# Kernel optimization log

Measured on AMD Instinct MI355X. Metric: run time of the kernel, lower is better.

The kernel has to match this reference:

```python
import jax, jax.numpy as jnp
from jax import lax
import numpy as np

EPS = 1e-5
ALPHA = 0.2  # LeakyReLU slope


def setup_inputs() -> dict:
    key = jax.random.key(0)
    ks = jax.random.split(key, 8)
    B, N, F_IN, HID, OUT, H = 32, 512, 256, 512, 512, 4
    D = OUT // H
    return {
        "x": jax.random.normal(ks[0], (B, N, F_IN), dtype=jnp.float32),
        "adj": jax.random.uniform(ks[1], (N, N), dtype=jnp.float32),
        "gc_w": jax.random.normal(ks[2], (F_IN, HID), dtype=jnp.float32) * 0.04,
        "gc_b": jax.random.normal(ks[3], (HID,), dtype=jnp.float32) * 0.04,
        "bn1_g": jnp.ones((HID,), jnp.float32),
        "bn1_b": jnp.zeros((HID,), jnp.float32),
        "bn1_m": jnp.zeros((HID,), jnp.float32),
        "bn1_v": jnp.ones((HID,), jnp.float32),
        "gat_w": jax.random.normal(ks[4], (H, D, HID), dtype=jnp.float32) * 0.04,
        "conv_w": jax.random.normal(ks[5], (OUT, OUT, 3), dtype=jnp.float32) * 0.02,
        "conv_b": jax.random.normal(ks[6], (OUT,), dtype=jnp.float32) * 0.02,
        "bn2_g": jnp.ones((OUT,), jnp.float32),
        "bn2_b": jnp.zeros((OUT,), jnp.float32),
        "bn2_m": jnp.zeros((OUT,), jnp.float32),
        "bn2_v": jnp.ones((OUT,), jnp.float32),
    }


def reference(x, adj, gc_w, gc_b, bn1_g, bn1_b, bn1_m, bn1_v, gat_w,
              conv_w, conv_b, bn2_g, bn2_b, bn2_m, bn2_v):
    # --- GraphConvolution: adj @ (x @ W) + b ---
    support = jnp.einsum('bnc,cd->bnd', x, gc_w)
    g = jnp.einsum('nm,bmd->bnd', adj, support) + gc_b  # [B,N,HID]
    # --- BatchNorm1d over channel dim (eval mode) + ReLU ---
    g = (g - bn1_m) * (bn1_g / jnp.sqrt(bn1_v + EPS)) + bn1_b
    g = jax.nn.relu(g)
    # --- Multi-head GAT (repeat/mul/sum == attention-weighted matmul) ---
    hh = jnp.einsum('bnf,hdf->bhnd', g, gat_w)           # per-head projections
    e = jnp.einsum('bhnd,bhmd->bhnm', hh, hh)            # logits [B,H,N,N]
    e = jnp.where(e > 0, e, ALPHA * e)                   # LeakyReLU
    att = jax.nn.softmax(e, axis=-1)
    o = jnp.einsum('bhnm,bhmd->bhnd', att, hh)
    B, H, N, D = o.shape
    o = o.transpose(0, 2, 1, 3).reshape(B, N, H * D)     # concat heads [B,N,OUT]
    # --- TCN block: conv1d(k=3,pad=1) over node axis + BN(eval) + ReLU ---
    xc = o.transpose(0, 2, 1)                            # [B,C,N]
    y = lax.conv_general_dilated(xc, conv_w, (1,), ((1, 1),),
                                 dimension_numbers=('NCH', 'OIH', 'NCH'))
    y = y + conv_b[None, :, None]
    y = (y - bn2_m[None, :, None]) * (bn2_g / jnp.sqrt(bn2_v + EPS))[None, :, None] + bn2_b[None, :, None]
    y = jax.nn.relu(y)
    return y.transpose(0, 2, 1)                          # [B,N,OUT]
```

## Files before the change

kernel.cpp:

```cpp
#include <hip/hip_runtime.h>
#include <math.h>

#define BATCH 32
#define NNODE 512
#define FIN   256
#define HIDC  512
#define OUTC  512
#define NHEAD 4
#define HDIM  128
#define EPSV  1e-5f
#define ALPHA_LR 0.2f

typedef _Float16 half8 __attribute__((ext_vector_type(8)));
typedef _Float16 half4v __attribute__((ext_vector_type(4)));
typedef float floatx4 __attribute__((ext_vector_type(4)));

#define GLOBAL_TO_LDS16(g, l)                                                  \
  __builtin_amdgcn_global_load_lds(                                            \
      (const __attribute__((address_space(1))) void*)(g),                      \
      (__attribute__((address_space(3))) void*)(l), 16, 0, 0)

__device__ __forceinline__ void split_gemm_acc(
    const _Float16* __restrict__ Ah, const _Float16* __restrict__ Al, int lda,
    const _Float16* __restrict__ Bh, const _Float16* __restrict__ Bl, int ldb,
    int K, int rowBase, int colBase,
    _Float16* sAh, _Float16* sAl, _Float16* sBh, _Float16* sBl,
    floatx4 acc[4][4], int tid) {
  const int lane = tid & 63, wave = tid >> 6;
  const int wr = (wave >> 1) * 64, wc = (wave & 1) * 64;
  const int fr = lane & 15, q = lane >> 4;
  const int r = tid >> 2, ko = (tid & 3) * 8;
  for (int k0 = 0; k0 < K; k0 += 32) {
    GLOBAL_TO_LDS16(&Ah[(size_t)(rowBase + r) * lda + k0 + ko], &sAh[tid * 8]);
    GLOBAL_TO_LDS16(&Ah[(size_t)(rowBase + r + 64) * lda + k0 + ko], &sAh[2048 + tid * 8]);
    GLOBAL_TO_LDS16(&Al[(size_t)(rowBase + r) * lda + k0 + ko], &sAl[tid * 8]);
    GLOBAL_TO_LDS16(&Al[(size_t)(rowBase + r + 64) * lda + k0 + ko], &sAl[2048 + tid * 8]);
    GLOBAL_TO_LDS16(&Bh[(size_t)(colBase + r) * ldb + k0 + ko], &sBh[tid * 8]);
    GLOBAL_TO_LDS16(&Bh[(size_t)(colBase + r + 64) * ldb + k0 + ko], &sBh[2048 + tid * 8]);
    GLOBAL_TO_LDS16(&Bl[(size_t)(colBase + r) * ldb + k0 + ko], &sBl[tid * 8]);
    GLOBAL_TO_LDS16(&Bl[(size_t)(colBase + r + 64) * ldb + k0 + ko], &sBl[2048 + tid * 8]);
    __syncthreads();
    half8 ah[4], al4[4], bh[4], bl4[4];
#pragma unroll
    for (int i = 0; i < 4; ++i) {
      ah[i]  = *(const half8*)&sAh[(wr + i * 16 + fr) * 32 + q * 8];
      al4[i] = *(const half8*)&sAl[(wr + i * 16 + fr) * 32 + q * 8];
    }
#pragma unroll
    for (int j = 0; j < 4; ++j) {
      bh[j]  = *(const half8*)&sBh[(wc + j * 16 + fr) * 32 + q * 8];
      bl4[j] = *(const half8*)&sBl[(wc + j * 16 + fr) * 32 + q * 8];
    }
#pragma unroll
    for (int i = 0; i < 4; ++i)
#pragma unroll
      for (int j = 0; j < 4; ++j) {
        acc[i][j] = __builtin_amdgcn_mfma_f32_16x16x32_f16(al4[i], bh[j], acc[i][j], 0, 0, 0);
        acc[i][j] = __builtin_amdgcn_mfma_f32_16x16x32_f16(ah[i], bl4[j], acc[i][j], 0, 0, 0);
        acc[i][j] = __builtin_amdgcn_mfma_f32_16x16x32_f16(ah[i], bh[j], acc[i][j], 0, 0, 0);
      }
    __syncthreads();
  }
}

__global__ __launch_bounds__(256) void k_prep(
    const float* __restrict__ adj, const float* __restrict__ gcw,
    const float* __restrict__ gatw, const float* __restrict__ cw,
    _Float16* __restrict__ ADJh, _Float16* __restrict__ ADJl,
    _Float16* __restrict__ GWh, _Float16* __restrict__ GWl,
    _Float16* __restrict__ GAh, _Float16* __restrict__ GAl,
    _Float16* __restrict__ WT, _Float16* __restrict__ OP) {
  const int i = blockIdx.x * 256 + threadIdx.x;
  if (i < 262144) {
    float v = adj[i];
    _Float16 h = (_Float16)v;
    ADJh[i] = h; ADJl[i] = (_Float16)(v - (float)h);
  } else if (i < 393216) {
    int j = i - 262144;
    int n = j >> 8, k = j & 255;
    float v = gcw[(size_t)k * HIDC + n];
    _Float16 h = (_Float16)v;
    GWh[j] = h; GWl[j] = (_Float16)(v - (float)h);
  } else if (i < 655360) {
    int j = i - 393216;
    float v = gatw[j];
    _Float16 h = (_Float16)v;
    GAh[j] = h; GAl[j] = (_Float16)(v - (float)h);
  } else if (i < 1441792) {
    int j = i - 655360;
    int n = j / 1536, kk = j - n * 1536;
    int tap = kk >> 9, ci = kk & 511;
    WT[j] = (_Float16)cw[(size_t)n * 1536 + ci * 3 + tap];
  } else if (i < 1474560) {
    int j = i - 1441792;
    int b = j >> 10, rs = (j >> 9) & 1, c = j & 511;
    OP[((size_t)b * 514 + rs * 513) * OUTC + c] = (_Float16)0.f;
  }
}

__global__ __launch_bounds__(256) void k_xsplit(const float* __restrict__ X,
                                                _Float16* __restrict__ Xh,
                                                _Float16* __restrict__ Xl) {
  const int i = (blockIdx.x * 256 + threadIdx.x) * 4;
  float4 v = *(const float4*)&X[i];
  half4v h, l;
  h[0] = (_Float16)v.x; l[0] = (_Float16)(v.x - (float)h[0]);
  h[1] = (_Float16)v.y; l[1] = (_Float16)(v.y - (float)h[1]);
  h[2] = (_Float16)v.z; l[2] = (_Float16)(v.z - (float)h[2]);
  h[3] = (_Float16)v.w; l[3] = (_Float16)(v.w - (float)h[3]);
  *(half4v*)&Xh[i] = h;
  *(half4v*)&Xl[i] = l;
}

__global__ __launch_bounds__(256) void k_support_t(
    const _Float16* __restrict__ GWh, const _Float16* __restrict__ GWl,
    const _Float16* __restrict__ Xh, const _Float16* __restrict__ Xl,
    _Float16* __restrict__ STh, _Float16* __restrict__ STl) {
  __shared__ _Float16 sm[4][4096];
  const int tid = threadIdx.x;
  const int rowBase = blockIdx.y * 128, colBase = blockIdx.x * 128;
  floatx4 acc[4][4] = {};
  split_gemm_acc(GWh, GWl, FIN, Xh, Xl, FIN, FIN, rowBase, colBase,
                 sm[0], sm[1], sm[2], sm[3], acc, tid);
  const int lane = tid & 63, wave = tid >> 6;
  const int wr = (wave >> 1) * 64, wc = (wave & 1) * 64;
  const int fr = lane & 15, q = lane >> 4;
#pragma unroll
  for (int i = 0; i < 4; ++i) {
    const int ch0 = rowBase + wr + i * 16 + q * 4;
#pragma unroll
    for (int rg = 0; rg < 4; ++rg) {
      size_t base = (size_t)(ch0 + rg) * 16384 + colBase + wc + fr;
#pragma unroll
      for (int j = 0; j < 4; ++j) {
        float v = acc[i][j][rg];
        _Float16 h = (_Float16)v;
        STh[base + j * 16] = h;
        STl[base + j * 16] = (_Float16)(v - (float)h);
      }
    }
  }
}

__global__ __launch_bounds__(256) void k_gcn(
    const _Float16* __restrict__ ADJh, const _Float16* __restrict__ ADJl,
    const _Float16* __restrict__ STh, const _Float16* __restrict__ STl,
    const float* __restrict__ gcb, const float* __restrict__ g1,
    const float* __restrict__ b1, const float* __restrict__ m1,
    const float* __restrict__ v1,
    _Float16* __restrict__ Gh, _Float16* __restrict__ Gl) {
  __shared__ _Float16 sm[4][4096];
  const int tid = threadIdx.x;
  const int rowBase = blockIdx.y * 128, colBase = blockIdx.x * 128;
  const int b = blockIdx.z;
  floatx4 acc[4][4] = {};
  split_gemm_acc(ADJh, ADJl, NNODE, STh + (size_t)b * NNODE, STl + (size_t)b * NNODE,
                 16384, NNODE, rowBase, colBase, sm[0], sm[1], sm[2], sm[3], acc, tid);
  const int lane = tid & 63, wave = tid >> 6;
  const int wr = (wave >> 1) * 64, wc = (wave & 1) * 64;
  const int fr = lane & 15, q = lane >> 4;
  float sc[4], of[4];
#pragma unroll
  for (int j = 0; j < 4; ++j) {
    int c = colBase + wc + j * 16 + fr;
    float s = g1[c] * rsqrtf(v1[c] + EPSV);
    sc[j] = s;
    of[j] = (gcb[c] - m1[c]) * s + b1[c];
  }
#pragma unroll
  for (int i = 0; i < 4; ++i) {
    const int n0 = rowBase + wr + i * 16 + q * 4;
#pragma unroll
    for (int rg = 0; rg < 4; ++rg) {
      size_t base = ((size_t)b * NNODE + n0 + rg) * HIDC + colBase + wc + fr;
#pragma unroll
      for (int j = 0; j < 4; ++j) {
        float v = fmaxf(fmaf(acc[i][j][rg], sc[j], of[j]), 0.0f);
        _Float16 h = (_Float16)v;
        Gh[base + j * 16] = h;
        Gl[base + j * 16] = (_Float16)(v - (float)h);
      }
    }
  }
}

__global__ __launch_bounds__(256) void k_hh(
    const _Float16* __restrict__ Gh, const _Float16* __restrict__ Gl,
    const _Float16* __restrict__ GAh, const _Float16* __restrict__ GAl,
    _Float16* __restrict__ HHh, _Float16* __restrict__ HHl) {
  __shared__ _Float16 sm[4][4096];
  const int tid = threadIdx.x;
  const int rowBase = blockIdx.y * 128, colBase = blockIdx.x * 128;
  floatx4 acc[4][4] = {};
  split_gemm_acc(Gh, Gl, HIDC, GAh, GAl, HIDC, HIDC, rowBase, colBase,
                 sm[0], sm[1], sm[2], sm[3], acc, tid);
  const int lane = tid & 63, wave = tid >> 6;
  const int wr = (wave >> 1) * 64, wc = (wave & 1) * 64;
  const int fr = lane & 15, q = lane >> 4;
#pragma unroll
  for (int i = 0; i < 4; ++i) {
    const int r0 = rowBase + wr + i * 16 + q * 4;
#pragma unroll
    for (int rg = 0; rg < 4; ++rg) {
      size_t base = (size_t)(r0 + rg) * OUTC + colBase + wc + fr;
#pragma unroll
      for (int j = 0; j < 4; ++j) {
        float v = acc[i][j][rg];
        _Float16 h = (_Float16)v;
        HHh[base + j * 16] = h;
        HHl[base + j * 16] = (_Float16)(v - (float)h);
      }
    }
  }
}

__global__ __launch_bounds__(256) void k_vt(const _Float16* __restrict__ HHh,
                                            _Float16* __restrict__ HHT) {
  __shared__ _Float16 sT[128 * 132];
  const int bt = blockIdx.x;
  const int nt = bt & 3, g = bt >> 2;
  const int bb = g >> 2, h = g & 3;
  const int tid = threadIdx.x;
  const int rr = tid >> 4, cc = (tid & 15) * 8;
#pragma unroll
  for (int it = 0; it < 8; ++it) {
    int node = rr + it * 16;
    half8 v = *(const half8*)&HHh[((size_t)bb * 512 + nt * 128 + node) * 512 + h * 128 + cc];
#pragma unroll
    for (int e = 0; e < 8; ++e) sT[(cc + e) * 132 + node] = v[e];
  }
  __syncthreads();
#pragma unroll
  for (int it = 0; it < 8; ++it) {
    int d = rr + it * 16;
    half8 v;
#pragma unroll
    for (int e = 0; e < 8; ++e) v[e] = sT[d * 132 + cc + e];
    *(half8*)&HHT[((size_t)g * 128 + d) * 512 + nt * 128 + cc] = v;
  }
}

__global__ __launch_bounds__(256, 3) void k_attn(
    const _Float16* __restrict__ HHh, const _Float16* __restrict__ HHl,
    const _Float16* __restrict__ HHT, _Float16* __restrict__ OP) {
  __shared__ _Float16 sK[8][2048];
  __shared__ _Float16 sP[64 * 68];
  _Float16* sV = &sK[0][0];
  const int tid = threadIdx.x;
  const int lane = tid & 63, wave = tid >> 6;
  const int fr = lane & 15, q = lane >> 4;
  const int id = blockIdx.x;
  const int slot = id >> 3;
  const int g = (id & 7) + 8 * (slot >> 3);
  const int qBase = (slot & 7) * 64;
  const int bb = g >> 2, h = g & 3;
  const int w16 = wave * 16;
  const _Float16* Qh = HHh + (size_t)bb * NNODE * OUTC + h * HDIM;
  const _Float16* Ql = HHl + (size_t)bb * NNODE * OUTC + h * HDIM;
  const _Float16* VT = HHT + (size_t)g * HDIM * NNODE;
  const int rk = tid >> 2, ck = (tid & 3) * 8;

  half8 qh[4], ql[4];
#pragma unroll
  for (int k0 = 0; k0 < 4; ++k0) {
    const size_t off = (size_t)(qBase + w16 + fr) * OUTC + k0 * 32 + q * 8;
    qh[k0] = *(const half8*)&Qh[off];
    ql[k0] = *(const half8*)&Ql[off];
  }

  floatx4 oacc[8] = {};
  float m_i[4], l_i[4];
#pragma unroll
  for (int rg = 0; rg < 4; ++rg) { m_i[rg] = -1e30f; l_i[rg] = 0.f; }

  for (int kt = 0; kt < 8; ++kt) {
    const int ktb = kt * 64;
#pragma unroll
    for (int t = 0; t < 4; ++t) {
      GLOBAL_TO_LDS16(&Qh[(size_t)(ktb + rk) * OUTC + t * 32 + ck], &sK[t][tid * 8]);
      GLOBAL_TO_LDS16(&Ql[(size_t)(ktb + rk) * OUTC + t * 32 + ck], &sK[4 + t][tid * 8]);
    }
    __syncthreads();
    floatx4 sacc[4] = {};
#pragma unroll
    for (int k0 = 0; k0 < 4; ++k0)
#pragma unroll
      for (int j = 0; j < 4; ++j) {
        half8 bh = *(const half8*)&sK[k0][(j * 16 + fr) * 32 + q * 8];
        half8 bl = *(const half8*)&sK[4 + k0][(j * 16 + fr) * 32 + q * 8];
        sacc[j] = __builtin_amdgcn_mfma_f32_16x16x32_f16(ql[k0], bh, sacc[j], 0, 0, 0);
        sacc[j] = __builtin_amdgcn_mfma_f32_16x16x32_f16(qh[k0], bl, sacc[j], 0, 0, 0);
        sacc[j] = __builtin_amdgcn_mfma_f32_16x16x32_f16(qh[k0], bh, sacc[j], 0, 0, 0);
      }
    __syncthreads();
#pragma unroll
    for (int j = 0; j < 4; ++j)
#pragma unroll
      for (int rg = 0; rg < 4; ++rg) {
        float v = sacc[j][rg];
        sacc[j][rg] = v > 0.f ? v : ALPHA_LR * v;
      }
#pragma unroll
    for (int rg = 0; rg < 4; ++rg) {
      float mx = sacc[0][rg];
#pragma unroll
      for (int j = 1; j < 4; ++j) mx = fmaxf(mx, sacc[j][rg]);
      mx = fmaxf(mx, __shfl_xor(mx, 1));
      mx = fmaxf(mx, __shfl_xor(mx, 2));
      mx = fmaxf(mx, __shfl_xor(mx, 4));
      mx = fmaxf(mx, __shfl_xor(mx, 8));
      float mnew = fmaxf(m_i[rg], mx);
      float alpha = __expf(m_i[rg] - mnew);
      m_i[rg] = mnew;
      float sum = 0.f;
#pragma unroll
      for (int j = 0; j < 4; ++j) {
        float p = __expf(sacc[j][rg] - mnew);
        sacc[j][rg] = p;
        sum += p;
      }
      sum += __shfl_xor(sum, 1);
      sum += __shfl_xor(sum, 2);
      sum += __shfl_xor(sum, 4);
      sum += __shfl_xor(sum, 8);
      l_i[rg] = l_i[rg] * alpha + sum;
#pragma unroll
      for (int j = 0; j < 8; ++j) oacc[j][rg] *= alpha;
    }
#pragma unroll
    for (int l = 0; l < 4; ++l)
      GLOBAL_TO_LDS16(&VT[(size_t)((l >> 1) * 64 + rk) * NNODE + ktb + (l & 1) * 32 + ck],
                      &sV[(l & 1) * 4096 + (l >> 1) * 2048 + tid * 8]);
#pragma unroll
    for (int j = 0; j < 4; ++j)
#pragma unroll
      for (int rg = 0; rg < 4; ++rg)
        sP[(w16 + q * 4 + rg) * 68 + j * 16 + fr] = (_Float16)sacc[j][rg];
    __syncthreads();
#pragma unroll
    for (int ks = 0; ks < 2; ++ks) {
      half8 pa = *(const half8*)&sP[(w16 + fr) * 68 + ks * 32 + q * 8];
#pragma unroll
      for (int j = 0; j < 8; ++j) {
        half8 bv = *(const half8*)&sV[ks * 4096 + (j * 16 + fr) * 32 + q * 8];
        oacc[j] = __builtin_amdgcn_mfma_f32_16x16x32_f16(pa, bv, oacc[j], 0, 0, 0);
      }
    }
    __syncthreads();
  }
#pragma unroll
  for (int rg = 0; rg < 4; ++rg) {
    const float inv = 1.0f / l_i[rg];
    const int node = qBase + w16 + q * 4 + rg;
    size_t base = ((size_t)bb * 514 + 1 + node) * OUTC + h * HDIM + fr;
#pragma unroll
    for (int j = 0; j < 8; ++j)
      OP[base + j * 16] = (_Float16)(oacc[j][rg] * inv);
  }
}

__global__ __launch_bounds__(256) void k_conv_mfma(
    const _Float16* __restrict__ OP, const _Float16* __restrict__ WT,
    const float* __restrict__ cb, const float* __restrict__ g2,
    const float* __restrict__ b2, const float* __restrict__ m2,
    const float* __restrict__ v2, float* __restrict__ Y) {
  __shared__ _Float16 At[128 * 32];
  __shared__ _Float16 Bt[128 * 32];
  const int tid = threadIdx.x;
  const int lane = tid & 63, wave = tid >> 6;
  const int wr = (wave >> 1) * 64, wc = (wave & 1) * 64;
  const int id = blockIdx.y * 4 + blockIdx.x;
  const int jj = id >> 3;
  const int rowBase = ((id & 7) * 16 + (jj >> 2)) * 128;
  const int colBase = (jj & 3) * 128;
  const int b = rowBase >> 9;
  const int n0 = rowBase & 511;
  const int r = tid >> 2;
  const int ko = (tid & 3) * 8;
  floatx4 acc[4][4] = {};
  for (int k0 = 0; k0 < 3 * OUTC; k0 += 32) {
    const int tap = k0 >> 9;
    const int cib = k0 & 511;
    const size_t abase = ((size_t)b * 514 + n0 + tap) * OUTC + cib + ko;
    GLOBAL_TO_LDS16(&OP[abase + (size_t)r * OUTC],        &At[tid * 8]);
    GLOBAL_TO_LDS16(&OP[abase + (size_t)(r + 64) * OUTC], &At[2048 + tid * 8]);
    GLOBAL_TO_LDS16(&WT[(size_t)(colBase + r) * 1536 + k0 + ko],      &Bt[tid * 8]);
    GLOBAL_TO_LDS16(&WT[(size_t)(colBase + r + 64) * 1536 + k0 + ko], &Bt[2048 + tid * 8]);
    __syncthreads();
    const int fr = lane & 15, q = lane >> 4;
    half8 af[4], bf[4];
#pragma unroll
    for (int i = 0; i < 4; ++i)
      af[i] = *(const half8*)&At[(wr + i * 16 + fr) * 32 + q * 8];
#pragma unroll
    for (int j = 0; j < 4; ++j)
      bf[j] = *(const half8*)&Bt[(wc + j * 16 + fr) * 32 + q * 8];
#pragma unroll
    for (int i = 0; i < 4; ++i)
#pragma unroll
      for (int j = 0; j < 4; ++j)
        acc[i][j] = __builtin_amdgcn_mfma_f32_16x16x32_f16(af[i], bf[j], acc[i][j], 0, 0, 0);
    __syncthreads();
  }
  const int fr = lane & 15, q = lane >> 4;
  float sc[4], of[4];
#pragma unroll
  for (int j = 0; j < 4; ++j) {
    int c = colBase + wc + j * 16 + fr;
    float s = g2[c] * rsqrtf(v2[c] + EPSV);
    sc[j] = s;
    of[j] = (cb[c] - m2[c]) * s + b2[c];
  }
#pragma unroll
  for (int i = 0; i < 4; ++i) {
    const int R0r = rowBase + wr + i * 16 + q * 4;
#pragma unroll
    for (int rg = 0; rg < 4; ++rg) {
      float* dst = &Y[(size_t)(R0r + rg) * OUTC + colBase + wc + fr];
#pragma unroll
      for (int j = 0; j < 4; ++j)
        dst[j * 16] = fmaxf(fmaf(acc[i][j][rg], sc[j], of[j]), 0.0f);
    }
  }
}

extern "C" void kernel_launch(void* const* d_in, const int* in_sizes, int n_in,
                              void* d_out, int out_size, void* d_ws, size_t ws_size,
                              hipStream_t stream) {
  const float* x     = (const float*)d_in[0];
  const float* adj   = (const float*)d_in[1];
  const float* gc_w  = (const float*)d_in[2];
  const float* gc_b  = (const float*)d_in[3];
  const float* bn1_g = (const float*)d_in[4];
  const float* bn1_b = (const float*)d_in[5];
  const float* bn1_m = (const float*)d_in[6];
  const float* bn1_v = (const float*)d_in[7];
  const float* gat_w = (const float*)d_in[8];
  const float* conv_w= (const float*)d_in[9];
  const float* conv_b= (const float*)d_in[10];
  const float* bn2_g = (const float*)d_in[11];
  const float* bn2_b = (const float*)d_in[12];
  const float* bn2_m = (const float*)d_in[13];
  const float* bn2_v = (const float*)d_in[14];
  float* out = (float*)d_out;

  char* ws = (char*)d_ws;
  _Float16* STh = (_Float16*)(ws + 0);
  _Float16* STl = (_Float16*)(ws + 16777216);
  _Float16* HHh = (_Float16*)(ws + 0);
  _Float16* HHl = (_Float16*)(ws + 16777216);
  _Float16* Xh  = (_Float16*)(ws + 33554432);
  _Float16* Xl  = (_Float16*)(ws + 41943040);
  _Float16* Gh  = (_Float16*)(ws + 33554432);
  _Float16* Gl  = (_Float16*)(ws + 50331648);
  _Float16* HHT = (_Float16*)(ws + 33554432);
  _Float16* OP  = (_Float16*)(ws + 67108864);
  _Float16* WT  = (_Float16*)(ws + 83951616);
  _Float16* ADJh= (_Float16*)(ws + 85524480);
  _Float16* ADJl= (_Float16*)(ws + 86048768);
  _Float16* GWh = (_Float16*)(ws + 86573056);
  _Float16* GWl = (_Float16*)(ws + 86835200);
  _Float16* GAh = (_Float16*)(ws + 87097344);
  _Float16* GAl = (_Float16*)(ws + 87621632);

  k_prep<<<5760, 256, 0, stream>>>(adj, gc_w, gat_w, conv_w,
                                   ADJh, ADJl, GWh, GWl, GAh, GAl, WT, OP);
  k_xsplit<<<4096, 256, 0, stream>>>(x, Xh, Xl);
  k_support_t<<<dim3(128, 4), 256, 0, stream>>>(GWh, GWl, Xh, Xl, STh, STl);
  k_gcn<<<dim3(4, 4, 32), 256, 0, stream>>>(ADJh, ADJl, STh, STl, gc_b,
                                            bn1_g, bn1_b, bn1_m, bn1_v, Gh, Gl);
  k_hh<<<dim3(4, 128), 256, 0, stream>>>(Gh, Gl, GAh, GAl, HHh, HHl);
  k_vt<<<512, 256, 0, stream>>>(HHh, HHT);
  k_attn<<<1024, 256, 0, stream>>>(HHh, HHl, HHT, OP);
  k_conv_mfma<<<dim3(4, 128), 256, 0, stream>>>(OP, WT, conv_b,
                                                bn2_g, bn2_b, bn2_m, bn2_v, out);
}
```

Measured before the change: 296.0 us.

## Prefetch next K tile during softmax and swizzle P tile in attention kernel

Splits the K staging buffer into hi and lo halves and issues the next tile's hi-part loads right after the QK^T MFMAs, so they overlap the softmax and PV stages. V is now staged into the lo-half buffer. The P scratch tile drops its padding in favour of an XOR swizzle to avoid LDS bank conflicts. The change also raises the launch-bounds occupancy hint to 4, adds s_setprio around MFMA sections, and replaces __syncthreads with raw barriers plus hand-written vmcnt waits. The manual waitcnt counts and buffer aliasing add correctness risk, and the tighter occupancy hint may cause register spills.

```diff
diff --git a/kernel.cpp b/kernel.cpp
--- a/kernel.cpp
+++ b/kernel.cpp
@@ -240,12 +240,13 @@
   }
 }
 
-__global__ __launch_bounds__(256, 3) void k_attn(
+__global__ __launch_bounds__(256, 4) void k_attn(
     const _Float16* __restrict__ HHh, const _Float16* __restrict__ HHl,
     const _Float16* __restrict__ HHT, _Float16* __restrict__ OP) {
-  __shared__ _Float16 sK[8][2048];
-  __shared__ _Float16 sP[64 * 68];
-  _Float16* sV = &sK[0][0];
+  __shared__ _Float16 sKhi[4][2048];
+  __shared__ _Float16 sKlo[4][2048];
+  __shared__ _Float16 sP[64 * 64];
+  _Float16* sV = &sKlo[0][0];
   const int tid = threadIdx.x;
   const int lane = tid & 63, wave = tid >> 6;
   const int fr = lane & 15, q = lane >> 4;
@@ -260,6 +261,11 @@
   const _Float16* VT = HHT + (size_t)g * HDIM * NNODE;
   const int rk = tid >> 2, ck = (tid & 3) * 8;
 
+#pragma unroll
+  for (int t = 0; t < 4; ++t) {
+    GLOBAL_TO_LDS16(&Qh[(size_t)rk * OUTC + t * 32 + ck], &sKhi[t][tid * 8]);
+    GLOBAL_TO_LDS16(&Ql[(size_t)rk * OUTC + t * 32 + ck], &sKlo[t][tid * 8]);
+  }
   half8 qh[4], ql[4];
 #pragma unroll
   for (int k0 = 0; k0 < 4; ++k0) {
@@ -267,32 +273,40 @@
     qh[k0] = *(const half8*)&Qh[off];
     ql[k0] = *(const half8*)&Ql[off];
   }
-
   floatx4 oacc[8] = {};
   float m_i[4], l_i[4];
 #pragma unroll
   for (int rg = 0; rg < 4; ++rg) { m_i[rg] = -1e30f; l_i[rg] = 0.f; }
+  __syncthreads();
 
   for (int kt = 0; kt < 8; ++kt) {
     const int ktb = kt * 64;
-#pragma unroll
-    for (int t = 0; t < 4; ++t) {
-      GLOBAL_TO_LDS16(&Qh[(size_t)(ktb + rk) * OUTC + t * 32 + ck], &sK[t][tid * 8]);
-      GLOBAL_TO_LDS16(&Ql[(size_t)(ktb + rk) * OUTC + t * 32 + ck], &sK[4 + t][tid * 8]);
-    }
-    __syncthreads();
     floatx4 sacc[4] = {};
+    __builtin_amdgcn_s_setprio(1);
 #pragma unroll
     for (int k0 = 0; k0 < 4; ++k0)
 #pragma unroll
       for (int j = 0; j < 4; ++j) {
-        half8 bh = *(const half8*)&sK[k0][(j * 16 + fr) * 32 + q * 8];
-        half8 bl = *(const half8*)&sK[4 + k0][(j * 16 + fr) * 32 + q * 8];
+        half8 bh = *(const half8*)&sKhi[k0][(j * 16 + fr) * 32 + q * 8];
+        half8 bl = *(const half8*)&sKlo[k0][(j * 16 + fr) * 32 + q * 8];
         sacc[j] = __builtin_amdgcn_mfma_f32_16x16x32_f16(ql[k0], bh, sacc[j], 0, 0, 0);
         sacc[j] = __builtin_amdgcn_mfma_f32_16x16x32_f16(qh[k0], bl, sacc[j], 0, 0, 0);
         sacc[j] = __builtin_amdgcn_mfma_f32_16x16x32_f16(qh[k0], bh, sacc[j], 0, 0, 0);
       }
-    __syncthreads();
+    __builtin_amdgcn_s_setprio(0);
+    asm volatile("" ::: "memory");
+    __builtin_amdgcn_s_barrier();
+    asm volatile("" ::: "memory");
+#pragma unroll
+    for (int l = 0; l < 4; ++l)
+      GLOBAL_TO_LDS16(&VT[(size_t)((l >> 1) * 64 + rk) * NNODE + ktb + (l & 1) * 32 + ck],
+                      &sV[(l & 1) * 4096 + (l >> 1) * 2048 + tid * 8]);
+    if (kt < 7) {
+#pragma unroll
+      for (int t = 0; t < 4; ++t)
+        GLOBAL_TO_LDS16(&Qh[(size_t)(ktb + 64 + rk) * OUTC + t * 32 + ck],
+                        &sKhi[t][tid * 8]);
+    }
 #pragma unroll
     for (int j = 0; j < 4; ++j)
 #pragma unroll
@@ -328,25 +342,41 @@
       for (int j = 0; j < 8; ++j) oacc[j][rg] *= alpha;
     }
 #pragma unroll
-    for (int l = 0; l < 4; ++l)
-      GLOBAL_TO_LDS16(&VT[(size_t)((l >> 1) * 64 + rk) * NNODE + ktb + (l & 1) * 32 + ck],
-                      &sV[(l & 1) * 4096 + (l >> 1) * 2048 + tid * 8]);
-#pragma unroll
     for (int j = 0; j < 4; ++j)
 #pragma unroll
-      for (int rg = 0; rg < 4; ++rg)
-        sP[(w16 + q * 4 + rg) * 68 + j * 16 + fr] = (_Float16)sacc[j][rg];
-    __syncthreads();
+      for (int rg = 0; rg < 4; ++rg) {
+        const int row = w16 + q * 4 + rg;
+        sP[row * 64 + (((j * 2 + (fr >> 3)) ^ (row & 7)) << 3) + (fr & 7)] =
+            (_Float16)sacc[j][rg];
+      }
+    if (kt < 7)
+      asm volatile("s_waitcnt vmcnt(4) lgkmcnt(0)" ::: "memory");
+    else
+      asm volatile("s_waitcnt vmcnt(0) lgkmcnt(0)" ::: "memory");
+    __builtin_amdgcn_s_barrier();
+    asm volatile("" ::: "memory");
+    __builtin_amdgcn_s_setprio(1);
 #pragma unroll
     for (int ks = 0; ks < 2; ++ks) {
-      half8 pa = *(const half8*)&sP[(w16 + fr) * 68 + ks * 32 + q * 8];
+      const int prow = w16 + fr;
+      half8 pa = *(const half8*)&sP[prow * 64 + (((ks * 4 + q) ^ (prow & 7)) << 3)];
 #pragma unroll
       for (int j = 0; j < 8; ++j) {
         half8 bv = *(const half8*)&sV[ks * 4096 + (j * 16 + fr) * 32 + q * 8];
         oacc[j] = __builtin_amdgcn_mfma_f32_16x16x32_f16(pa, bv, oacc[j], 0, 0, 0);
       }
     }
-    __syncthreads();
+    __builtin_amdgcn_s_setprio(0);
+    if (kt < 7) {
+      asm volatile("" ::: "memory");
+      __builtin_amdgcn_s_barrier();
+      asm volatile("" ::: "memory");
+#pragma unroll
+      for (int t = 0; t < 4; ++t)
+        GLOBAL_TO_LDS16(&Ql[(size_t)(ktb + 64 + rk) * OUTC + t * 32 + ck],
+                        &sKlo[t][tid * 8]);
+      __syncthreads();
+    }
   }
 #pragma unroll
   for (int rg = 0; rg < 4; ++rg) {
```

After: 311.9 us. 1.05x slower.
